# Performance work log

Measured on AMD Instinct MI355X. Metric: run time of the kernel, lower is better.

Reference implementation:

```python
import jax, jax.numpy as jnp
import numpy as np

N_NODES = 100000
N_EDGES = 800000
H = 128
MAX_Z = 1000
N_GRAPHS = 500  # batch = repeat(arange(500), 200); subgraphs are contiguous


def setup_inputs() -> dict:
    key = jax.random.key(0)
    ks = jax.random.split(key, 16)
    z = jax.random.randint(ks[0], (N_NODES,), 0, MAX_Z)
    edge_index = jax.random.randint(ks[1], (2, N_EDGES), 0, N_NODES)
    batch = jnp.repeat(jnp.arange(N_GRAPHS), N_NODES // N_GRAPHS)
    edge_mask = jax.random.randint(ks[2], (N_EDGES,), 0, 2).astype(bool)
    s = 1.0 / np.sqrt(H)
    inp = {
        "z": z, "edge_index": edge_index, "batch": batch, "edge_mask": edge_mask,
        "z_table": jax.random.normal(ks[3], (MAX_Z, H), dtype=jnp.float32) * 0.02,
        "W0": jax.random.uniform(ks[4], (H, H), minval=-s, maxval=s),
        "b0": jax.random.uniform(ks[5], (H,), minval=-s, maxval=s),
        "W1": jax.random.uniform(ks[6], (H, H), minval=-s, maxval=s),
        "b1": jax.random.uniform(ks[7], (H,), minval=-s, maxval=s),
        "W2": jax.random.uniform(ks[8], (H, H), minval=-s, maxval=s),
        "b2": jax.random.uniform(ks[9], (H,), minval=-s, maxval=s),
        "lin1_w": jax.random.uniform(ks[10], (H, H), minval=-s, maxval=s),
        "lin1_b": jax.random.uniform(ks[11], (H,), minval=-s, maxval=s),
        "lin2_w": jax.random.uniform(ks[12], (H, 1), minval=-s, maxval=s),
        "lin2_b": jax.random.uniform(ks[13], (1,), minval=-s, maxval=s),
    }
    return inp


def _gcn_conv(x, W, b, src, dst, w):
    # PyG GCNConv with self-loops (fill=1) and symmetric normalization.
    xw = x @ W                                                # [N,H]
    deg = jax.ops.segment_sum(w, dst, num_segments=N_NODES) + 1.0
    dinv = jax.lax.rsqrt(deg)                                 # deg >= 1 (self-loop)
    coef = (dinv[src] * w * dinv[dst])[:, None]               # [E,1]
    out = jax.ops.segment_sum(coef * xw[src], dst, num_segments=N_NODES)
    out = out + (dinv * dinv)[:, None] * xw                   # self-loop messages
    return out + b


def reference(z, edge_index, batch, edge_mask, z_table,
              W0, b0, W1, b1, W2, b2, lin1_w, lin1_b, lin2_w, lin2_b):
    x = z_table[z]                                            # z embedding, [N,H]
    src, dst = edge_index[0], edge_index[1]
    # fuse='minus': edge_index[:, edge_mask] == zero-weight masked-out edges
    w = edge_mask.astype(x.dtype)
    x = jax.nn.relu(_gcn_conv(x, W0, b0, src, dst, w))        # dropout: eval mode
    x = jax.nn.relu(_gcn_conv(x, W1, b1, src, dst, w))
    x = _gcn_conv(x, W2, b2, src, dst, w)
    # hadamard pooling: first two nodes of each (sorted, contiguous) subgraph
    center = jnp.searchsorted(batch, jnp.arange(N_GRAPHS))
    x = x[center] * x[center + 1]                             # [G,H]
    x = jax.nn.relu(x @ lin1_w + lin1_b)
    return x @ lin2_w + lin2_b                                # [G,1]
```

## Files before the change

### kernel.cpp

```cpp
#include <hip/hip_runtime.h>

#define N_NODES 100000
#define N_EDGES 800000
#define H 128
#define N_GRAPHS 500
#define ELL_CAP 32
#define NB 391
#define MAXC1 33008
#define NC_ROWS 1008
#define CTR0 0
#define CTR1 64
#define LA_GRID 2080
#define LB_GRID 1040

typedef __attribute__((ext_vector_type(8))) short bf16x8;
typedef __attribute__((ext_vector_type(4))) float f32x4;

__device__ __forceinline__ unsigned short f2bf(float f) {
    union { float f; unsigned u; } x; x.f = f;
    unsigned r = x.u + 0x7fffu + ((x.u >> 16) & 1u);
    return (unsigned short)(r >> 16);
}
__device__ __forceinline__ float bf2f(unsigned short u) {
    return __uint_as_float((unsigned)u << 16);
}

__global__ void k_setup(int* fill, int* f0, int* f1, int* ctrs,
                        const float* W0, const float* W1, const float* W2,
                        unsigned short* Wp) {
    int b = blockIdx.x;
    if (b < NB) {
        int i = b * 256 + threadIdx.x;
        if (i < N_NODES) { fill[i] = 0; f0[i] = 0; f1[i] = 0; }
        if (i < 128) ctrs[i] = 0;
    } else {
        int bb = b - NB;
        int wi = bb >> 3;
        const float* W = (wi == 0) ? W0 : (wi == 1) ? W1 : W2;
        int t = (bb & 7) * 256 + threadIdx.x;
        int lane = t & 63, kt = (t >> 6) & 3, c = t >> 8;
        int quad = lane >> 4, n = c * 16 + (lane & 15);
        unsigned short o[8];
#pragma unroll
        for (int j = 0; j < 8; j++)
            o[j] = f2bf(W[(kt * 32 + quad * 8 + j) * H + n]);
        ushort4 lo = { o[0], o[1], o[2], o[3] }, hi = { o[4], o[5], o[6], o[7] };
        unsigned short* dst = Wp + (size_t)wi * 16384 + (size_t)t * 8;
        *(ushort4*)(dst)     = lo;
        *(ushort4*)(dst + 4) = hi;
    }
}

__global__ void k_edge(const int* src, const int* dst, const int* mask,
                       int* fill, int* ell) {
    int e = blockIdx.x * 256 + threadIdx.x;
    if (e >= N_EDGES) return;
    if (!mask[e]) return;
    int d = dst[e];
    int p = atomicAdd(&fill[d], 1);
    if (p < ELL_CAP) ell[(size_t)d * ELL_CAP + p] = src[e];
}

__global__ void k_n1(const int* fill, const int* ell, int* f1, int* f0,
                     int* list1, int* list0, int* ctrs) {
    __shared__ int wtot[4];
    __shared__ int bbase0, bbase1;
    int tid = threadIdx.x, lane = tid & 63, wv = tid >> 6;
    int c = blockIdx.x * 4 + wv;
    int s = -1;
    if (c < 2 * N_GRAPHS) {
        int v = (c >> 1) * 200 + (c & 1);
        int n = fill[v]; if (n > ELL_CAP) n = ELL_CAP;
        s = (lane < n) ? ell[(size_t)v * ELL_CAP + lane] : ((lane == n) ? v : -1);
    }
    bool need = false;
    if (s >= 0 && atomicExch(&f1[s], 1) == 0) {
        f0[s] = 1;
        need = true;
    }
    unsigned long long b = __ballot(need);
    int total = __popcll(b);
    int pre = __popcll(b & ((1ull << lane) - 1ull));
    if (lane == 0) wtot[wv] = total;
    __syncthreads();
    if (tid == 0) {
        int bt = wtot[0] + wtot[1] + wtot[2] + wtot[3];
        if (bt) {
            bbase1 = atomicAdd(&ctrs[CTR1], bt);
            bbase0 = atomicAdd(&ctrs[CTR0], bt);
        }
    }
    __syncthreads();
    if (need) {
        int off = pre;
        for (int w2 = 0; w2 < 4; w2++) if (w2 < wv) off += wtot[w2];
        list1[bbase1 + off] = s;
        list0[bbase0 + off] = s;
    }
}

__global__ void k_n0(const int* fill, const int* ell, const int* list1,
                     int* f0, int* list0, int* ctrs) {
    __shared__ int wtot[4];
    __shared__ int bbase;
    int tid = threadIdx.x, lane = tid & 63, wv = tid >> 6;
    int i = blockIdx.x * 4 + wv;
    int cnt1 = ctrs[CTR1];
    bool need = false;
    int s = 0;
    if (i < cnt1) {
        int v = list1[i];
        int n = fill[v]; if (n > ELL_CAP) n = ELL_CAP;
        if (lane < n) {
            s = ell[(size_t)v * ELL_CAP + lane];
            need = (atomicExch(&f0[s], 1) == 0);
        }
    }
    unsigned long long b = __ballot(need);
    int total = __popcll(b);
    int pre = __popcll(b & ((1ull << lane) - 1ull));
    if (lane == 0) wtot[wv] = total;
    __syncthreads();
    if (tid == 0) {
        int bt = wtot[0] + wtot[1] + wtot[2] + wtot[3];
        if (bt) bbase = atomicAdd(&ctrs[CTR0], bt);
    }
    __syncthreads();
    if (need) {
        int off = pre;
        for (int w2 = 0; w2 < 4; w2++) if (w2 < wv) off += wtot[w2];
        list0[bbase + off] = s;
    }
}

__global__ __launch_bounds__(256) void k_layerA(const int* z, const float* tab,
                                                const int* ell, const int* fill,
                                                const int* list, const int* countp,
                                                const unsigned short* Wp,
                                                const float* bias,
                                                unsigned short* xb) {
    __shared__ unsigned short yt[16][136];
    int count = *countp;
    int tid = threadIdx.x, lane = tid & 63, wv = tid >> 6;
    int l2 = lane * 2;
    int m = lane & 15, quad = lane >> 4;

    for (int t = blockIdx.x; t * 16 < count; t += LA_GRID) {
        for (int q = 0; q < 4; q++) {
            int r = t * 16 + wv * 4 + q;
            float ax = 0.f, ay = 0.f;
            if (r < count) {
                int v = list[r];
                int ntrue = fill[v];
                int n = ntrue > ELL_CAP ? ELL_CAP : ntrue;
                float dv = rsqrtf(1.0f + (float)ntrue);
                int px = (lane < n) ? ell[(size_t)v * ELL_CAP + lane] : 0;
                float pc = 0.f;
                if (lane < n) pc = rsqrtf(1.0f + (float)fill[px]) * dv;
                float sc = dv * dv;
                float2 xs = *(const float2*)(tab + (size_t)z[v] * H + l2);
                ax = sc * xs.x; ay = sc * xs.y;
                int k = 0;
                for (; k + 3 < n; k += 4) {
                    int s0 = __shfl(px, k),   s1 = __shfl(px, k + 1);
                    int s2 = __shfl(px, k + 2), s3 = __shfl(px, k + 3);
                    float c0 = __shfl(pc, k),   c1 = __shfl(pc, k + 1);
                    float c2 = __shfl(pc, k + 2), c3 = __shfl(pc, k + 3);
                    int z0 = z[s0], z1 = z[s1], z2 = z[s2], z3 = z[s3];
                    float2 m0 = *(const float2*)(tab + (size_t)z0 * H + l2);
                    float2 m1 = *(const float2*)(tab + (size_t)z1 * H + l2);
                    float2 m2 = *(const float2*)(tab + (size_t)z2 * H + l2);
                    float2 m3 = *(const float2*)(tab + (size_t)z3 * H + l2);
                    ax += c0 * m0.x + c1 * m1.x + c2 * m2.x + c3 * m3.x;
                    ay += c0 * m0.y + c1 * m1.y + c2 * m2.y + c3 * m3.y;
                }
                for (; k < n; k++) {
                    int s = __shfl(px, k); float c = __shfl(pc, k);
                    float2 m0 = *(const float2*)(tab + (size_t)z[s] * H + l2);
                    ax += c * m0.x; ay += c * m0.y;
                }
            }
            ushort2 o; o.x = f2bf(ax); o.y = f2bf(ay);
            *(ushort2*)&yt[wv * 4 + q][l2] = o;
        }
        __syncthreads();

        bf16x8 a0 = *(const bf16x8*)&yt[m][quad * 8];
        bf16x8 a1 = *(const bf16x8*)&yt[m][32 + quad * 8];
        bf16x8 a2 = *(const bf16x8*)&yt[m][64 + quad * 8];
        bf16x8 a3 = *(const bf16x8*)&yt[m][96 + quad * 8];

        f32x4 acc[2];
#pragma unroll
        for (int c2 = 0; c2 < 2; c2++) {
            int c = wv * 2 + c2;
            const unsigned short* bp = Wp + ((size_t)(c * 4) * 64 + lane) * 8;
            bf16x8 b0 = *(const bf16x8*)(bp);
            bf16x8 b1 = *(const bf16x8*)(bp + 64 * 8);
            bf16x8 b2 = *(const bf16x8*)(bp + 128 * 8);
            bf16x8 b3 = *(const bf16x8*)(bp + 192 * 8);
            f32x4 a = (f32x4){0.f, 0.f, 0.f, 0.f};
            a = __builtin_amdgcn_mfma_f32_16x16x32_bf16(a0, b0, a, 0, 0, 0);
            a = __builtin_amdgcn_mfma_f32_16x16x32_bf16(a1, b1, a, 0, 0, 0);
            a = __builtin_amdgcn_mfma_f32_16x16x32_bf16(a2, b2, a, 0, 0, 0);
            a = __builtin_amdgcn_mfma_f32_16x16x32_bf16(a3, b3, a, 0, 0, 0);
            acc[c2] = a;
        }

        int r0 = t * 16 + quad * 4;
        int rid[4];
#pragma unroll
        for (int i = 0; i < 4; i++) {
            int r = r0 + i;
            rid[i] = (r < count) ? list[r] : -1;
        }
#pragma unroll
        for (int c2 = 0; c2 < 2; c2++) {
            int col = (wv * 2 + c2) * 16 + m;
            float bv = bias[col];
#pragma unroll
            for (int i = 0; i < 4; i++)
                if (rid[i] >= 0)
                    xb[(size_t)rid[i] * H + col] = f2bf(fmaxf(acc[c2][i] + bv, 0.f));
        }
        __syncthreads();
    }
}

__global__ __launch_bounds__(256) void k_layerB(const unsigned short* xin,
                                                const int* ell, const int* fill,
                                                const int* list, const int* countp,
                                                const unsigned short* Wp,
                                                const float* bias,
                                                unsigned short* xout) {
    __shared__ unsigned short yt[16][136];
    int count = *countp;
    int tid = threadIdx.x, lane = tid & 63, wv = tid >> 6;
    int l2 = lane * 2;
    int m = lane & 15, quad = lane >> 4;

    for (int t = blockIdx.x; t * 16 < count; t += LB_GRID) {
        for (int q = 0; q < 4; q++) {
            int r = t * 16 + wv * 4 + q;
            float ax = 0.f, ay = 0.f;
            if (r < count) {
                int v = list[r];
                int ntrue = fill[v];
                int n = ntrue > ELL_CAP ? ELL_CAP : ntrue;
                float dv = rsqrtf(1.0f + (float)ntrue);
                int px = (lane < n) ? ell[(size_t)v * ELL_CAP + lane] : 0;
                float pc = 0.f;
                if (lane < n) pc = rsqrtf(1.0f + (float)fill[px]) * dv;
                float sc = dv * dv;
                ushort2 xs = *(const ushort2*)(xin + (size_t)v * H + l2);
                ax = sc * bf2f(xs.x); ay = sc * bf2f(xs.y);
                int k = 0;
                for (; k + 3 < n; k += 4) {
                    int s0 = __shfl(px, k),   s1 = __shfl(px, k + 1);
                    int s2 = __shfl(px, k + 2), s3 = __shfl(px, k + 3);
                    float c0 = __shfl(pc, k),   c1 = __shfl(pc, k + 1);
                    float c2 = __shfl(pc, k + 2), c3 = __shfl(pc, k + 3);
                    ushort2 m0 = *(const ushort2*)(xin + (size_t)s0 * H + l2);
                    ushort2 m1 = *(const ushort2*)(xin + (size_t)s1 * H + l2);
                    ushort2 m2 = *(const ushort2*)(xin + (size_t)s2 * H + l2);
                    ushort2 m3 = *(const ushort2*)(xin + (size_t)s3 * H + l2);
                    ax += c0 * bf2f(m0.x) + c1 * bf2f(m1.x) + c2 * bf2f(m2.x) + c3 * bf2f(m3.x);
                    ay += c0 * bf2f(m0.y) + c1 * bf2f(m1.y) + c2 * bf2f(m2.y) + c3 * bf2f(m3.y);
                }
                for (; k < n; k++) {
                    int s = __shfl(px, k); float c = __shfl(pc, k);
                    ushort2 m0 = *(const ushort2*)(xin + (size_t)s * H + l2);
                    ax += c * bf2f(m0.x); ay += c * bf2f(m0.y);
                }
            }
            ushort2 o; o.x = f2bf(ax); o.y = f2bf(ay);
            *(ushort2*)&yt[wv * 4 + q][l2] = o;
        }
        __syncthreads();

        bf16x8 a0 = *(const bf16x8*)&yt[m][quad * 8];
        bf16x8 a1 = *(const bf16x8*)&yt[m][32 + quad * 8];
        bf16x8 a2 = *(const bf16x8*)&yt[m][64 + quad * 8];
        bf16x8 a3 = *(const bf16x8*)&yt[m][96 + quad * 8];

        f32x4 acc[2];
#pragma unroll
        for (int c2 = 0; c2 < 2; c2++) {
            int c = wv * 2 + c2;
            const unsigned short* bp = Wp + ((size_t)(c * 4) * 64 + lane) * 8;
            bf16x8 b0 = *(const bf16x8*)(bp);
            bf16x8 b1 = *(const bf16x8*)(bp + 64 * 8);
            bf16x8 b2 = *(const bf16x8*)(bp + 128 * 8);
            bf16x8 b3 = *(const bf16x8*)(bp + 192 * 8);
            f32x4 a = (f32x4){0.f, 0.f, 0.f, 0.f};
            a = __builtin_amdgcn_mfma_f32_16x16x32_bf16(a0, b0, a, 0, 0, 0);
            a = __builtin_amdgcn_mfma_f32_16x16x32_bf16(a1, b1, a, 0, 0, 0);
            a = __builtin_amdgcn_mfma_f32_16x16x32_bf16(a2, b2, a, 0, 0, 0);
            a = __builtin_amdgcn_mfma_f32_16x16x32_bf16(a3, b3, a, 0, 0, 0);
            acc[c2] = a;
        }

        int r0 = t * 16 + quad * 4;
        int rid[4];
#pragma unroll
        for (int i = 0; i < 4; i++) {
            int r = r0 + i;
            rid[i] = (r < count) ? list[r] : -1;
        }
#pragma unroll
        for (int c2 = 0; c2 < 2; c2++) {
            int col = (wv * 2 + c2) * 16 + m;
            float bv = bias[col];
#pragma unroll
            for (int i = 0; i < 4; i++)
                if (rid[i] >= 0)
                    xout[(size_t)rid[i] * H + col] = f2bf(fmaxf(acc[c2][i] + bv, 0.f));
        }
        __syncthreads();
    }
}

__global__ __launch_bounds__(256) void k_layer2(const unsigned short* xin,
                                                const int* ell, const int* fill,
                                                const unsigned short* Wp,
                                                const float* b2,
                                                const float* l1w, const float* l1b,
                                                const float* l2w, const float* l2b,
                                                float* out) {
    __shared__ unsigned short yt[16][136];
    __shared__ float ct[16][132];
    int t = blockIdx.x;
    int tid = threadIdx.x, lane = tid & 63, wv = tid >> 6;
    int l2 = lane * 2;

    for (int q = 0; q < 4; q++) {
        int idx = t * 16 + wv * 4 + q;
        float ax = 0.f, ay = 0.f;
        if (idx < 2 * N_GRAPHS) {
            int v = (idx >> 1) * 200 + (idx & 1);
            int ntrue = fill[v];
            int n = ntrue > ELL_CAP ? ELL_CAP : ntrue;
            float dv = rsqrtf(1.0f + (float)ntrue);
            int px = (lane < n) ? ell[(size_t)v * ELL_CAP + lane] : 0;
            float pc = 0.f;
            if (lane < n) pc = rsqrtf(1.0f + (float)fill[px]) * dv;
            float sc = dv * dv;
            ushort2 xs = *(const ushort2*)(xin + (size_t)v * H + l2);
            ax = sc * bf2f(xs.x); ay = sc * bf2f(xs.y);
            for (int k = 0; k < n; k++) {
                int s = __shfl(px, k); float c = __shfl(pc, k);
                ushort2 m0 = *(const ushort2*)(xin + (size_t)s * H + l2);
                ax += c * bf2f(m0.x); ay += c * bf2f(m0.y);
            }
        }
        ushort2 o; o.x = f2bf(ax); o.y = f2bf(ay);
        *(ushort2*)&yt[wv * 4 + q][l2] = o;
    }
    __syncthreads();

    int m = lane & 15, quad = lane >> 4;
    bf16x8 a0 = *(const bf16x8*)&yt[m][quad * 8];
    bf16x8 a1 = *(const bf16x8*)&yt[m][32 + quad * 8];
    bf16x8 a2 = *(const bf16x8*)&yt[m][64 + quad * 8];
    bf16x8 a3 = *(const bf16x8*)&yt[m][96 + quad * 8];

#pragma unroll
    for (int c2 = 0; c2 < 2; c2++) {
        int c = wv * 2 + c2;
        const unsigned short* bp = Wp + ((size_t)(c * 4) * 64 + lane) * 8;
        bf16x8 b0 = *(const bf16x8*)(bp);
        bf16x8 b1 = *(const bf16x8*)(bp + 64 * 8);
        bf16x8 bb = *(const bf16x8*)(bp + 128 * 8);
        bf16x8 b3 = *(const bf16x8*)(bp + 192 * 8);
        f32x4 a = (f32x4){0.f, 0.f, 0.f, 0.f};
        a = __builtin_amdgcn_mfma_f32_16x16x32_bf16(a0, b0, a, 0, 0, 0);
        a = __builtin_amdgcn_mfma_f32_16x16x32_bf16(a1, b1, a, 0, 0, 0);
        a = __builtin_amdgcn_mfma_f32_16x16x32_bf16(a2, bb, a, 0, 0, 0);
        a = __builtin_amdgcn_mfma_f32_16x16x32_bf16(a3, b3, a, 0, 0, 0);
        int col = c * 16 + m;
        float bv = b2[col];
#pragma unroll
        for (int i = 0; i < 4; i++)
            ct[quad * 4 + i][col] = a[i] + bv;
    }
    __syncthreads();

    int gl = tid >> 5, jq = tid & 31, j4 = jq * 4;
    int g = t * 8 + gl;
    float4 h = *(const float4*)(l1b + j4);
    const float* r0 = &ct[2 * gl][0];
    const float* r1 = &ct[2 * gl + 1][0];
#pragma unroll 4
    for (int k = 0; k < H; k++) {
        float pk = r0[k] * r1[k];
        float4 wv4 = *(const float4*)(l1w + (size_t)k * H + j4);
        h.x += pk * wv4.x; h.y += pk * wv4.y;
        h.z += pk * wv4.z; h.w += pk * wv4.w;
    }
    float4 l2v = *(const float4*)(l2w + j4);
    float s = fmaxf(h.x, 0.f) * l2v.x + fmaxf(h.y, 0.f) * l2v.y +
              fmaxf(h.z, 0.f) * l2v.z + fmaxf(h.w, 0.f) * l2v.w;
#pragma unroll
    for (int d = 16; d > 0; d >>= 1) s += __shfl_xor(s, d, 32);
    if (jq == 0 && g < N_GRAPHS) out[g] = s + l2b[0];
}

extern "C" void kernel_launch(void* const* d_in, const int* in_sizes, int n_in,
                              void* d_out, int out_size, void* d_ws, size_t ws_size,
                              hipStream_t stream) {
    const int*   z    = (const int*)d_in[0];
    const int*   esrc = (const int*)d_in[1];
    const int*   edst = ((const int*)d_in[1]) + N_EDGES;
    const int*   mask = (const int*)d_in[3];
    const float* ztab = (const float*)d_in[4];
    const float* W0   = (const float*)d_in[5];
    const float* b0   = (const float*)d_in[6];
    const float* W1   = (const float*)d_in[7];
    const float* b1   = (const float*)d_in[8];
    const float* W2   = (const float*)d_in[9];
    const float* b2   = (const float*)d_in[10];
    const float* l1w  = (const float*)d_in[11];
    const float* l1b  = (const float*)d_in[12];
    const float* l2w  = (const float*)d_in[13];
    const float* l2b  = (const float*)d_in[14];
    float* out = (float*)d_out;

    char* w = (char*)d_ws;
    size_t o = 0;
    auto carve = [&](size_t bytes) { char* p = w + o; o = (o + bytes + 255) & ~(size_t)255; return p; };
    unsigned short* xb    = (unsigned short*)carve((size_t)N_NODES * H * 2);
    unsigned short* xc    = (unsigned short*)carve((size_t)N_NODES * H * 2);
    int*            fill  = (int*)carve((size_t)N_NODES * 4);
    int*            ell   = (int*)carve((size_t)N_NODES * ELL_CAP * 4);
    int*            f0    = (int*)carve((size_t)N_NODES * 4);
    int*            f1    = (int*)carve((size_t)N_NODES * 4);
    int*            list0 = (int*)carve((size_t)N_NODES * 4);
    int*            list1 = (int*)carve((size_t)MAXC1 * 4);
    int*            ctrs  = (int*)carve(512);
    unsigned short* Wp    = (unsigned short*)carve((size_t)3 * 16384 * 2);

    k_setup<<<NB + 24, 256, 0, stream>>>(fill, f0, f1, ctrs, W0, W1, W2, Wp);
    k_edge <<<(N_EDGES + 255) / 256, 256, 0, stream>>>(esrc, edst, mask, fill, ell);
    k_n1   <<<(2 * N_GRAPHS + 3) / 4, 256, 0, stream>>>(fill, ell, f1, f0, list1, list0, ctrs);
    k_n0   <<<(MAXC1 + 3) / 4, 256, 0, stream>>>(fill, ell, list1, f0, list0, ctrs);

    k_layerA<<<LA_GRID, 256, 0, stream>>>(z, ztab, ell, fill, list0,
                                          &ctrs[CTR0], Wp, b0, xb);
    k_layerB<<<LB_GRID, 256, 0, stream>>>(xb, ell, fill, list1, &ctrs[CTR1],
                                          Wp + 16384, b1, xc);
    k_layer2<<<NC_ROWS / 16, 256, 0, stream>>>(xc, ell, fill, Wp + 32768, b2,
                                               l1w, l1b, l2w, l2b, out);
}
```

Before: 182.9 us.

## Use bf16 embedding table, 512-thread layer blocks, prefetch z, unroll layer2 gather

The embedding table is converted to bf16 once in the setup kernel, so layer A gathers half the bytes. Neighbour z indices are now loaded in parallel per lane before the loop rather than inside it. Layers A and B move to 512-thread blocks with 8 waves, each wave aggregating 2 rows and computing one 16-column MFMA tile, which spreads the serial gather work over more waves. The final layer's gather loop is unrolled by 4. The bf16 table adds rounding to the first-layer inputs, and larger blocks may lower occupancy.

```diff
diff --git a/kernel.cpp b/kernel.cpp
--- a/kernel.cpp
+++ b/kernel.cpp
@@ -3,9 +3,11 @@
 #define N_NODES 100000
 #define N_EDGES 800000
 #define H 128
+#define MAX_Z 1000
 #define N_GRAPHS 500
 #define ELL_CAP 32
 #define NB 391
+#define TB 125
 #define MAXC1 33008
 #define NC_ROWS 1008
 #define CTR0 0
@@ -27,13 +29,14 @@
 
 __global__ void k_setup(int* fill, int* f0, int* f1, int* ctrs,
                         const float* W0, const float* W1, const float* W2,
-                        unsigned short* Wp) {
+                        unsigned short* Wp, const float* ztab,
+                        unsigned short* tabb) {
     int b = blockIdx.x;
     if (b < NB) {
         int i = b * 256 + threadIdx.x;
         if (i < N_NODES) { fill[i] = 0; f0[i] = 0; f1[i] = 0; }
         if (i < 128) ctrs[i] = 0;
-    } else {
+    } else if (b < NB + 24) {
         int bb = b - NB;
         int wi = bb >> 3;
         const float* W = (wi == 0) ? W0 : (wi == 1) ? W1 : W2;
@@ -48,6 +51,13 @@
         unsigned short* dst = Wp + (size_t)wi * 16384 + (size_t)t * 8;
         *(ushort4*)(dst)     = lo;
         *(ushort4*)(dst + 4) = hi;
+    } else {
+        int i = (b - NB - 24) * 256 + threadIdx.x;
+        if (i < MAX_Z * H / 4) {
+            float4 v = *(const float4*)(ztab + (size_t)i * 4);
+            ushort4 o = { f2bf(v.x), f2bf(v.y), f2bf(v.z), f2bf(v.w) };
+            *(ushort4*)(tabb + (size_t)i * 4) = o;
+        }
     }
 }
 
@@ -133,7 +143,8 @@
     }
 }
 
-__global__ __launch_bounds__(256) void k_layerA(const int* z, const float* tab,
+__global__ __launch_bounds__(512) void k_layerA(const int* z,
+                                                const unsigned short* tabb,
                                                 const int* ell, const int* fill,
                                                 const int* list, const int* countp,
                                                 const unsigned short* Wp,
@@ -146,8 +157,8 @@
     int m = lane & 15, quad = lane >> 4;
 
     for (int t = blockIdx.x; t * 16 < count; t += LA_GRID) {
-        for (int q = 0; q < 4; q++) {
-            int r = t * 16 + wv * 4 + q;
+        for (int q = 0; q < 2; q++) {
+            int r = t * 16 + wv * 2 + q;
             float ax = 0.f, ay = 0.f;
             if (r < count) {
                 int v = list[r];
@@ -155,33 +166,35 @@
                 int n = ntrue > ELL_CAP ? ELL_CAP : ntrue;
                 float dv = rsqrtf(1.0f + (float)ntrue);
                 int px = (lane < n) ? ell[(size_t)v * ELL_CAP + lane] : 0;
-                float pc = 0.f;
-                if (lane < n) pc = rsqrtf(1.0f + (float)fill[px]) * dv;
+                int zx = 0; float pc = 0.f;
+                if (lane < n) {
+                    zx = z[px];
+                    pc = rsqrtf(1.0f + (float)fill[px]) * dv;
+                }
                 float sc = dv * dv;
-                float2 xs = *(const float2*)(tab + (size_t)z[v] * H + l2);
-                ax = sc * xs.x; ay = sc * xs.y;
+                ushort2 xs = *(const ushort2*)(tabb + (size_t)z[v] * H + l2);
+                ax = sc * bf2f(xs.x); ay = sc * bf2f(xs.y);
                 int k = 0;
                 for (; k + 3 < n; k += 4) {
-                    int s0 = __shfl(px, k),   s1 = __shfl(px, k + 1);
-                    int s2 = __shfl(px, k + 2), s3 = __shfl(px, k + 3);
+                    int z0 = __shfl(zx, k),   z1 = __shfl(zx, k + 1);
+                    int z2 = __shfl(zx, k + 2), z3 = __shfl(zx, k + 3);
                     float c0 = __shfl(pc, k),   c1 = __shfl(pc, k + 1);
                     float c2 = __shfl(pc, k + 2), c3 = __shfl(pc, k + 3);
-                    int z0 = z[s0], z1 = z[s1], z2 = z[s2], z3 = z[s3];
-                    float2 m0 = *(const float2*)(tab + (size_t)z0 * H + l2);
-                    float2 m1 = *(const float2*)(tab + (size_t)z1 * H + l2);
-                    float2 m2 = *(const float2*)(tab + (size_t)z2 * H + l2);
-                    float2 m3 = *(const float2*)(tab + (size_t)z3 * H + l2);
-                    ax += c0 * m0.x + c1 * m1.x + c2 * m2.x + c3 * m3.x;
-                    ay += c0 * m0.y + c1 * m1.y + c2 * m2.y + c3 * m3.y;
+                    ushort2 m0 = *(const ushort2*)(tabb + (size_t)z0 * H + l2);
+                    ushort2 m1 = *(const ushort2*)(tabb + (size_t)z1 * H + l2);
+                    ushort2 m2 = *(const ushort2*)(tabb + (size_t)z2 * H + l2);
+                    ushort2 m3 = *(const ushort2*)(tabb + (size_t)z3 * H + l2);
+                    ax += c0 * bf2f(m0.x) + c1 * bf2f(m1.x) + c2 * bf2f(m2.x) + c3 * bf2f(m3.x);
+                    ay += c0 * bf2f(m0.y) + c1 * bf2f(m1.y) + c2 * bf2f(m2.y) + c3 * bf2f(m3.y);
                 }
                 for (; k < n; k++) {
-                    int s = __shfl(px, k); float c = __shfl(pc, k);
-                    float2 m0 = *(const float2*)(tab + (size_t)z[s] * H + l2);
-                    ax += c * m0.x; ay += c * m0.y;
+                    int zz = __shfl(zx, k); float c = __shfl(pc, k);
+                    ushort2 m0 = *(const ushort2*)(tabb + (size_t)zz * H + l2);
+                    ax += c * bf2f(m0.x); ay += c * bf2f(m0.y);
                 }
             }
             ushort2 o; o.x = f2bf(ax); o.y = f2bf(ay);
-            *(ushort2*)&yt[wv * 4 + q][l2] = o;
+            *(ushort2*)&yt[wv * 2 + q][l2] = o;
         }
         __syncthreads();
 
@@ -189,45 +202,31 @@
         bf16x8 a1 = *(const bf16x8*)&yt[m][32 + quad * 8];
         bf16x8 a2 = *(const bf16x8*)&yt[m][64 + quad * 8];
         bf16x8 a3 = *(const bf16x8*)&yt[m][96 + quad * 8];
-
-        f32x4 acc[2];
-#pragma unroll
-        for (int c2 = 0; c2 < 2; c2++) {
-            int c = wv * 2 + c2;
-            const unsigned short* bp = Wp + ((size_t)(c * 4) * 64 + lane) * 8;
-            bf16x8 b0 = *(const bf16x8*)(bp);
-            bf16x8 b1 = *(const bf16x8*)(bp + 64 * 8);
-            bf16x8 b2 = *(const bf16x8*)(bp + 128 * 8);
-            bf16x8 b3 = *(const bf16x8*)(bp + 192 * 8);
-            f32x4 a = (f32x4){0.f, 0.f, 0.f, 0.f};
-            a = __builtin_amdgcn_mfma_f32_16x16x32_bf16(a0, b0, a, 0, 0, 0);
-            a = __builtin_amdgcn_mfma_f32_16x16x32_bf16(a1, b1, a, 0, 0, 0);
-            a = __builtin_amdgcn_mfma_f32_16x16x32_bf16(a2, b2, a, 0, 0, 0);
-            a = __builtin_amdgcn_mfma_f32_16x16x32_bf16(a3, b3, a, 0, 0, 0);
-            acc[c2] = a;
-        }
+        const unsigned short* bp = Wp + ((size_t)(wv * 4) * 64 + lane) * 8;
+        bf16x8 b0 = *(const bf16x8*)(bp);
+        bf16x8 b1 = *(const bf16x8*)(bp + 64 * 8);
+        bf16x8 b2 = *(const bf16x8*)(bp + 128 * 8);
+        bf16x8 b3 = *(const bf16x8*)(bp + 192 * 8);
+        f32x4 a = (f32x4){0.f, 0.f, 0.f, 0.f};
+        a = __builtin_amdgcn_mfma_f32_16x16x32_bf16(a0, b0, a, 0, 0, 0);
+        a = __builtin_amdgcn_mfma_f32_16x16x32_bf16(a1, b1, a, 0, 0, 0);
+        a = __builtin_amdgcn_mfma_f32_16x16x32_bf16(a2, b2, a, 0, 0, 0);
+        a = __builtin_amdgcn_mfma_f32_16x16x32_bf16(a3, b3, a, 0, 0, 0);
 
         int r0 = t * 16 + quad * 4;
-        int rid[4];
+        int col = wv * 16 + m;
+        float bv = bias[col];
 #pragma unroll
         for (int i = 0; i < 4; i++) {
             int r = r0 + i;
-            rid[i] = (r < count) ? list[r] : -1;
-        }
-#pragma unroll
-        for (int c2 = 0; c2 < 2; c2++) {
-            int col = (wv * 2 + c2) * 16 + m;
-            float bv = bias[col];
-#pragma unroll
-            for (int i = 0; i < 4; i++)
-                if (rid[i] >= 0)
-                    xb[(size_t)rid[i] * H + col] = f2bf(fmaxf(acc[c2][i] + bv, 0.f));
+            if (r < count)
+                xb[(size_t)list[r] * H + col] = f2bf(fmaxf(a[i] + bv, 0.f));
         }
         __syncthreads();
     }
 }
 
-__global__ __launch_bounds__(256) void k_layerB(const unsigned short* xin,
+__global__ __launch_bounds__(512) void k_layerB(const unsigned short* xin,
                                                 const int* ell, const int* fill,
                                                 const int* list, const int* countp,
                                                 const unsigned short* Wp,
@@ -240,8 +239,8 @@
     int m = lane & 15, quad = lane >> 4;
 
     for (int t = blockIdx.x; t * 16 < count; t += LB_GRID) {
-        for (int q = 0; q < 4; q++) {
-            int r = t * 16 + wv * 4 + q;
+        for (int q = 0; q < 2; q++) {
+            int r = t * 16 + wv * 2 + q;
             float ax = 0.f, ay = 0.f;
             if (r < count) {
                 int v = list[r];
@@ -274,7 +273,7 @@
                 }
             }
             ushort2 o; o.x = f2bf(ax); o.y = f2bf(ay);
-            *(ushort2*)&yt[wv * 4 + q][l2] = o;
+            *(ushort2*)&yt[wv * 2 + q][l2] = o;
         }
         __syncthreads();
 
@@ -282,39 +281,25 @@
         bf16x8 a1 = *(const bf16x8*)&yt[m][32 + quad * 8];
         bf16x8 a2 = *(const bf16x8*)&yt[m][64 + quad * 8];
         bf16x8 a3 = *(const bf16x8*)&yt[m][96 + quad * 8];
-
-        f32x4 acc[2];
-#pragma unroll
-        for (int c2 = 0; c2 < 2; c2++) {
-            int c = wv * 2 + c2;
-            const unsigned short* bp = Wp + ((size_t)(c * 4) * 64 + lane) * 8;
-            bf16x8 b0 = *(const bf16x8*)(bp);
-            bf16x8 b1 = *(const bf16x8*)(bp + 64 * 8);
-            bf16x8 b2 = *(const bf16x8*)(bp + 128 * 8);
-            bf16x8 b3 = *(const bf16x8*)(bp + 192 * 8);
-            f32x4 a = (f32x4){0.f, 0.f, 0.f, 0.f};
-            a = __builtin_amdgcn_mfma_f32_16x16x32_bf16(a0, b0, a, 0, 0, 0);
-            a = __builtin_amdgcn_mfma_f32_16x16x32_bf16(a1, b1, a, 0, 0, 0);
-            a = __builtin_amdgcn_mfma_f32_16x16x32_bf16(a2, b2, a, 0, 0, 0);
-            a = __builtin_amdgcn_mfma_f32_16x16x32_bf16(a3, b3, a, 0, 0, 0);
-            acc[c2] = a;
-        }
+        const unsigned short* bp = Wp + ((size_t)(wv * 4) * 64 + lane) * 8;
+        bf16x8 b0 = *(const bf16x8*)(bp);
+        bf16x8 b1 = *(const bf16x8*)(bp + 64 * 8);
+        bf16x8 b2 = *(const bf16x8*)(bp + 128 * 8);
+        bf16x8 b3 = *(const bf16x8*)(bp + 192 * 8);
+        f32x4 a = (f32x4){0.f, 0.f, 0.f, 0.f};
+        a = __builtin_amdgcn_mfma_f32_16x16x32_bf16(a0, b0, a, 0, 0, 0);
+        a = __builtin_amdgcn_mfma_f32_16x16x32_bf16(a1, b1, a, 0, 0, 0);
+        a = __builtin_amdgcn_mfma_f32_16x16x32_bf16(a2, b2, a, 0, 0, 0);
+        a = __builtin_amdgcn_mfma_f32_16x16x32_bf16(a3, b3, a, 0, 0, 0);
 
         int r0 = t * 16 + quad * 4;
-        int rid[4];
+        int col = wv * 16 + m;
+        float bv = bias[col];
 #pragma unroll
         for (int i = 0; i < 4; i++) {
             int r = r0 + i;
-            rid[i] = (r < count) ? list[r] : -1;
-        }
-#pragma unroll
-        for (int c2 = 0; c2 < 2; c2++) {
-            int col = (wv * 2 + c2) * 16 + m;
-            float bv = bias[col];
-#pragma unroll
-            for (int i = 0; i < 4; i++)
-                if (rid[i] >= 0)
-                    xout[(size_t)rid[i] * H + col] = f2bf(fmaxf(acc[c2][i] + bv, 0.f));
+            if (r < count)
+                xout[(size_t)list[r] * H + col] = f2bf(fmaxf(a[i] + bv, 0.f));
         }
         __syncthreads();
     }
@@ -347,7 +332,20 @@
             float sc = dv * dv;
             ushort2 xs = *(const ushort2*)(xin + (size_t)v * H + l2);
             ax = sc * bf2f(xs.x); ay = sc * bf2f(xs.y);
-            for (int k = 0; k < n; k++) {
+            int k = 0;
+            for (; k + 3 < n; k += 4) {
+                int s0 = __shfl(px, k),   s1 = __shfl(px, k + 1);
+                int s2 = __shfl(px, k + 2), s3 = __shfl(px, k + 3);
+                float c0 = __shfl(pc, k),   c1 = __shfl(pc, k + 1);
+                float c2 = __shfl(pc, k + 2), c3 = __shfl(pc, k + 3);
+                ushort2 m0 = *(const ushort2*)(xin + (size_t)s0 * H + l2);
+                ushort2 m1 = *(const ushort2*)(xin + (size_t)s1 * H + l2);
+                ushort2 m2 = *(const ushort2*)(xin + (size_t)s2 * H + l2);
+                ushort2 m3 = *(const ushort2*)(xin + (size_t)s3 * H + l2);
+                ax += c0 * bf2f(m0.x) + c1 * bf2f(m1.x) + c2 * bf2f(m2.x) + c3 * bf2f(m3.x);
+                ay += c0 * bf2f(m0.y) + c1 * bf2f(m1.y) + c2 * bf2f(m2.y) + c3 * bf2f(m3.y);
+            }
+            for (; k < n; k++) {
                 int s = __shfl(px, k); float c = __shfl(pc, k);
                 ushort2 m0 = *(const ushort2*)(xin + (size_t)s * H + l2);
                 ax += c * bf2f(m0.x); ay += c * bf2f(m0.y);
@@ -438,15 +436,17 @@
     int*            list1 = (int*)carve((size_t)MAXC1 * 4);
     int*            ctrs  = (int*)carve(512);
     unsigned short* Wp    = (unsigned short*)carve((size_t)3 * 16384 * 2);
-
-    k_setup<<<NB + 24, 256, 0, stream>>>(fill, f0, f1, ctrs, W0, W1, W2, Wp);
+    unsigned short* tabb  = (unsigned short*)carve((size_t)MAX_Z * H * 2);
+
+    k_setup<<<NB + 24 + TB, 256, 0, stream>>>(fill, f0, f1, ctrs,
+                                              W0, W1, W2, Wp, ztab, tabb);
     k_edge <<<(N_EDGES + 255) / 256, 256, 0, stream>>>(esrc, edst, mask, fill, ell);
     k_n1   <<<(2 * N_GRAPHS + 3) / 4, 256, 0, stream>>>(fill, ell, f1, f0, list1, list0, ctrs);
     k_n0   <<<(MAXC1 + 3) / 4, 256, 0, stream>>>(fill, ell, list1, f0, list0, ctrs);
 
-    k_layerA<<<LA_GRID, 256, 0, stream>>>(z, ztab, ell, fill, list0,
+    k_layerA<<<LA_GRID, 512, 0, stream>>>(z, tabb, ell, fill, list0,
                                           &ctrs[CTR0], Wp, b0, xb);
-    k_layerB<<<LB_GRID, 256, 0, stream>>>(xb, ell, fill, list1, &ctrs[CTR1],
+    k_layerB<<<LB_GRID, 512, 0, stream>>>(xb, ell, fill, list1, &ctrs[CTR1],
                                           Wp + 16384, b1, xc);
     k_layer2<<<NC_ROWS / 16, 256, 0, stream>>>(xc, ell, fill, Wp + 32768, b2,
                                                l1w, l1b, l2w, l2b, out);
```

Measured after the change: 173.9 us. -4.9%, faster.
